# Kernel tuning notes

Hardware: AMD Instinct MI355X
Metric: run time of the kernel (lower is better)

The kernel has to match this reference:

```python
import jax, jax.numpy as jnp
import numpy as np


def setup_inputs() -> dict:
    key = jax.random.key(0)
    k1, k2 = jax.random.split(key)
    n_nodes, n_feat, n_edges = 100000, 64, 1600000
    x = jax.random.normal(k1, (n_nodes, n_feat), dtype=jnp.float32)
    edge_index = jax.random.randint(k2, (2, n_edges), 0, n_nodes, dtype=jnp.int64)
    return {"x": x, "edge_index": edge_index}


def reference(x, edge_index):
    # Faithful JAX version of OneHopGCNNormNodeLabelAggregator.forward:
    #   adj = SparseTensor.from_edge_index(edge_index)  (values = 1)
    #   adj_norm = gcn_norm(adj)  -> add self-loops (diag=1), symmetric D^-1/2 A D^-1/2
    #   x_neighbors = adj_norm.t() @ x
    n = x.shape[0]
    self_loops = jnp.arange(n, dtype=edge_index.dtype)
    row = jnp.concatenate([edge_index[0], self_loops])  # source of adj entry A[row, col]
    col = jnp.concatenate([edge_index[1], self_loops])
    # degree over rows (sparsesum dim=1 after fill_diag)
    deg = jax.ops.segment_sum(jnp.ones(row.shape, x.dtype), row, num_segments=n)
    deg_inv_sqrt = jnp.where(deg > 0, jax.lax.rsqrt(deg), 0.0).astype(x.dtype)
    # symmetric norm weight per edge
    w = deg_inv_sqrt[row] * deg_inv_sqrt[col]  # [E+n]
    # adj_norm.t() @ x : out[col] += w * x[row]
    x_neighbors = jax.ops.segment_sum(w[:, None] * x[row], col, num_segments=n)
    return x_neighbors
```

## Files before the change

kernel.cpp:

```cpp
#include <hip/hip_runtime.h>

#define NFEAT 64
#define BSHIFT 8
#define BCOLS 256
#define NBMAX 512
#define CAP 5120
#define CHUNK 4096
#define PT 512
#define NITP (CHUNK / PT)
#define FT 512
#define UT 512
#define FBIT (CAP / UT)


__device__ __forceinline__ unsigned short f2bf(float f) {
    unsigned int u = __float_as_uint(f);
    return (unsigned short)((u + 0x7FFFu + ((u >> 16) & 1u)) >> 16);
}

__device__ __forceinline__ float bflo(unsigned int u) {
    return __uint_as_float(u << 16);
}
__device__ __forceinline__ float bfhi(unsigned int u) {
    return __uint_as_float(u & 0xFFFF0000u);
}

__device__ __forceinline__ int wave_incl_scan(int v, int lane) {
    #pragma unroll
    for (int off = 1; off < 64; off <<= 1) {
        int u = __shfl_up(v, off);
        if (lane >= off) v += u;
    }
    return v;
}

__global__ void k_init(int* __restrict__ bcur, int* __restrict__ bcurR) {
    int t = threadIdx.x;
    bcur[t]  = t * CAP;
    bcurR[t] = t * CAP;
}

__global__ __launch_bounds__(PT)
void k_partCR(const int* __restrict__ rows, const int* __restrict__ cols,
              int* __restrict__ bcur, int* __restrict__ bcurR,
              int* __restrict__ part, unsigned char* __restrict__ partR, int E) {
    __shared__ int histC[NBMAX];
    __shared__ int histR[NBMAX];
    __shared__ int gbaseC[NBMAX];
    __shared__ int gbaseR[NBMAX];
    __shared__ int wsumC[8];
    __shared__ int wsumR[8];
    __shared__ int stageC[CHUNK];
    __shared__ unsigned char stageR[CHUNK];
    __shared__ unsigned short bidC[CHUNK];
    __shared__ unsigned short bidR[CHUNK];
    int chunk0 = blockIdx.x * CHUNK;
    int cnt = min(CHUNK, E - chunk0);
    int t = threadIdx.x;
    int lane = t & 63, wid = t >> 6;

    histC[t] = 0; histR[t] = 0;
    __syncthreads();

    int pk[NITP];
    unsigned char rpk[NITP];
    unsigned short cb[NITP], rb[NITP];
    #pragma unroll
    for (int k = 0; k < NITP; k++) {
        int i = t + k * PT;
        if (i < cnt) {
            int c = cols[chunk0 + i];
            int r = rows[chunk0 + i];
            int b  = c >> BSHIFT;
            int b2 = r >> BSHIFT;
            pk[k]  = ((c & (BCOLS - 1)) << 17) | r;
            rpk[k] = (unsigned char)(r & (BCOLS - 1));
            cb[k] = (unsigned short)b;
            rb[k] = (unsigned short)b2;
            atomicAdd(&histC[b], 1);
            atomicAdd(&histR[b2], 1);
        }
    }
    __syncthreads();

    int v1 = histC[t];
    int inc1 = wave_incl_scan(v1, lane);
    if (lane == 63) wsumC[wid] = inc1;
    int v2 = histR[t];
    int inc2 = wave_incl_scan(v2, lane);
    if (lane == 63) wsumR[wid] = inc2;
    __syncthreads();
    int addC = 0, addR = 0;
    #pragma unroll
    for (int k = 0; k < 8; k++) {
        if (k < wid) { addC += wsumC[k]; addR += wsumR[k]; }
    }
    int exC = inc1 - v1 + addC;
    int exR = inc2 - v2 + addR;
    gbaseC[t] = (v1 > 0) ? (atomicAdd(&bcur[t], v1) - exC) : 0;
    gbaseR[t] = (v2 > 0) ? (atomicAdd(&bcurR[t], v2) - exR) : 0;
    histC[t] = exC;
    histR[t] = exR;
    __syncthreads();

    #pragma unroll
    for (int k = 0; k < NITP; k++) {
        int i = t + k * PT;
        if (i < cnt) {
            int p = atomicAdd(&histC[cb[k]], 1);
            stageC[p] = pk[k];
            bidC[p] = cb[k];
            int p2 = atomicAdd(&histR[rb[k]], 1);
            stageR[p2] = rpk[k];
            bidR[p2] = rb[k];
        }
    }
    __syncthreads();
    for (int p = t; p < cnt; p += PT) {
        int b = bidC[p];
        int idx = gbaseC[b] + p;
        if (idx < (b + 1) * CAP) part[idx] = stageC[p];
        int b2 = bidR[p];
        int idx2 = gbaseR[b2] + p;
        if (idx2 < (b2 + 1) * CAP) partR[idx2] = stageR[p];
    }
}

__global__ __launch_bounds__(FT)
void k_fillR(const unsigned char* __restrict__ partR, const int* __restrict__ bcurR,
             const float4* __restrict__ x4, float* __restrict__ dinv,
             ushort4* __restrict__ xs4, int n) {
    __shared__ int lcnt[BCOLS];
    __shared__ float ldinv[BCOLS];
    int b = blockIdx.x;
    int s = b * CAP;
    int t = threadIdx.x;

    int cntR = min(bcurR[b] - s, CAP);
    if (t < BCOLS) lcnt[t] = 0;
    __syncthreads();
    for (int i = t; i < cntR; i += FT)
        atomicAdd(&lcnt[partR[s + i]], 1);
    __syncthreads();
    if (t < BCOLS) {
        float d = rsqrtf((float)(lcnt[t] + 1));
        ldinv[t] = d;
        int gr = (b << BSHIFT) + t;
        if (gr < n) dinv[gr] = d;
    }
    __syncthreads();
    size_t base4 = (size_t)(b << BSHIFT) << 4;
    int lim = min(BCOLS, n - (b << BSHIFT)) << 4;
    for (int i = t; i < lim; i += FT) {
        float dd = ldinv[i >> 4];
        float4 vv = x4[base4 + i];
        ushort4 o;
        o.x = f2bf(dd * vv.x); o.y = f2bf(dd * vv.y);
        o.z = f2bf(dd * vv.z); o.w = f2bf(dd * vv.w);
        xs4[base4 + i] = o;
    }
}

__global__ __launch_bounds__(UT)
void k_fuse(const int* __restrict__ part, const int* __restrict__ bcur,
            const unsigned short* __restrict__ xs,
            const float* __restrict__ dinv,
            float4* __restrict__ out4, int n) {
    __shared__ int lcnt[BCOLS];
    __shared__ int lps[BCOLS];
    __shared__ int cur[BCOLS];
    __shared__ int wsum[4];
    __shared__ int stage[CAP];
    int b = blockIdx.x;
    int s = b * CAP;
    int cnt = min(bcur[b] - s, CAP);
    int t = threadIdx.x;
    int lane = t & 63, wid = t >> 6;

    if (t < BCOLS) lcnt[t] = 0;
    __syncthreads();

    int pk[FBIT];
    #pragma unroll
    for (int k = 0; k < FBIT; k++) {
        int i = t + k * UT;
        if (i < cnt) {
            int v2 = part[s + i];
            pk[k] = v2;
            atomicAdd(&lcnt[v2 >> 17], 1);
        }
    }
    __syncthreads();

    int v = 0, inc = 0;
    if (t < BCOLS) {
        v = lcnt[t];
        inc = wave_incl_scan(v, lane);
        if (lane == 63) wsum[wid] = inc;
    }
    __syncthreads();
    if (t < BCOLS) {
        int add = 0;
        if (wid > 0) add += wsum[0];
        if (wid > 1) add += wsum[1];
        if (wid > 2) add += wsum[2];
        int ex = inc - v + add;
        lps[t] = ex;
        cur[t] = ex;
    }
    __syncthreads();

    #pragma unroll
    for (int k = 0; k < FBIT; k++) {
        int i = t + k * UT;
        if (i < cnt) {
            int v2 = pk[k];
            int p = atomicAdd(&cur[v2 >> 17], 1);
            stage[p] = v2 & 0x1FFFF;
        }
    }
    __syncthreads();

    int gg = t >> 3, li = t & 7;
    #pragma unroll
    for (int cc = 0; cc < BCOLS; cc += 64) {
        int c = cc + gg;
        int node = (b << BSHIFT) + c;
        if (node < n) {
            int ss = lps[c];
            int len = lcnt[c];
            float a0 = 0.f, a1 = 0.f, a2 = 0.f, a3 = 0.f;
            float a4 = 0.f, a5 = 0.f, a6 = 0.f, a7 = 0.f;
            int npair = len >> 1;
            uint4 u0, u1;
            if (npair > 0) {
                int r0 = stage[ss], r1 = stage[ss + 1];
                u0 = *((const uint4*)(xs + ((size_t)r0 << 6)) + li);
                u1 = *((const uint4*)(xs + ((size_t)r1 << 6)) + li);
            }
            for (int q = 1; q < npair; q++) {
                int p = ss + q * 2;
                int r0 = stage[p], r1 = stage[p + 1];
                uint4 n0 = *((const uint4*)(xs + ((size_t)r0 << 6)) + li);
                uint4 n1 = *((const uint4*)(xs + ((size_t)r1 << 6)) + li);
                a0 += bflo(u0.x); a1 += bfhi(u0.x);
                a2 += bflo(u0.y); a3 += bfhi(u0.y);
                a4 += bflo(u0.z); a5 += bfhi(u0.z);
                a6 += bflo(u0.w); a7 += bfhi(u0.w);
                a0 += bflo(u1.x); a1 += bfhi(u1.x);
                a2 += bflo(u1.y); a3 += bfhi(u1.y);
                a4 += bflo(u1.z); a5 += bfhi(u1.z);
                a6 += bflo(u1.w); a7 += bfhi(u1.w);
                u0 = n0; u1 = n1;
            }
            if (npair > 0) {
                a0 += bflo(u0.x); a1 += bfhi(u0.x);
                a2 += bflo(u0.y); a3 += bfhi(u0.y);
                a4 += bflo(u0.z); a5 += bfhi(u0.z);
                a6 += bflo(u0.w); a7 += bfhi(u0.w);
                a0 += bflo(u1.x); a1 += bfhi(u1.x);
                a2 += bflo(u1.y); a3 += bfhi(u1.y);
                a4 += bflo(u1.z); a5 += bfhi(u1.z);
                a6 += bflo(u1.w); a7 += bfhi(u1.w);
            }
            if (len & 1) {
                int r = stage[ss + len - 1];
                uint4 u = *((const uint4*)(xs + ((size_t)r << 6)) + li);
                a0 += bflo(u.x); a1 += bfhi(u.x);
                a2 += bflo(u.y); a3 += bfhi(u.y);
                a4 += bflo(u.z); a5 += bfhi(u.z);
                a6 += bflo(u.w); a7 += bfhi(u.w);
            }
            float dc = dinv[node];
            uint4 us = *((const uint4*)(xs + ((size_t)node << 6)) + li);
            float4 r0o, r1o;
            r0o.x = dc * (a0 + bflo(us.x));
            r0o.y = dc * (a1 + bfhi(us.x));
            r0o.z = dc * (a2 + bflo(us.y));
            r0o.w = dc * (a3 + bfhi(us.y));
            r1o.x = dc * (a4 + bflo(us.z));
            r1o.y = dc * (a5 + bfhi(us.z));
            r1o.z = dc * (a6 + bflo(us.w));
            r1o.w = dc * (a7 + bfhi(us.w));
            size_t ob = ((size_t)node << 4) + (li << 1);
            out4[ob] = r0o;
            out4[ob + 1] = r1o;
        }
    }
}

extern "C" void kernel_launch(void* const* d_in, const int* in_sizes, int n_in,
                              void* d_out, int out_size, void* d_ws, size_t ws_size,
                              hipStream_t stream) {
    const float* x    = (const float*)d_in[0];
    const int*   eidx = (const int*)d_in[1];

    const int n = in_sizes[0] / NFEAT;
    const int E = in_sizes[1] / 2;
    const int* rows = eidx;
    const int* cols = eidx + E;
    float* out = (float*)d_out;

    const int nbuck = (n + BCOLS - 1) >> BSHIFT;

    char* w = (char*)d_ws;
    int*   bcur  = (int*)w;     w += NBMAX * 4;
    int*   bcurR = (int*)w;     w += NBMAX * 4;
    float* dinv  = (float*)w;   w += (size_t)n * 4;
    w = (char*)(((uintptr_t)w + 15) & ~(uintptr_t)15);
    unsigned short* xs = (unsigned short*)w;  w += (size_t)n * NFEAT * 2;
    int*   part  = (int*)w;     w += (size_t)nbuck * CAP * 4;
    unsigned char* partR = (unsigned char*)w;

    k_init<<<1, NBMAX, 0, stream>>>(bcur, bcurR);

    int nchunk = (E + CHUNK - 1) / CHUNK;
    k_partCR<<<nchunk, PT, 0, stream>>>(rows, cols, bcur, bcurR, part, partR, E);
    k_fillR<<<nbuck, FT, 0, stream>>>(partR, bcurR, (const float4*)x,
                                      dinv, (ushort4*)xs, n);
    k_fuse<<<nbuck, UT, 0, stream>>>(part, bcur, xs, dinv,
                                     (float4*)out, n);
}
```

Baseline: 140.5 us.

## Replace shared-memory atomics with wave ballot match-based histogram and ranking

Replaces per-element LDS atomicAdd in the partition, degree-count and bucket-sort kernels with a ballot-based key-matching scheme. Each wave computes an equality mask over the bucket bits, keeps per-wave histograms, and places each element by its rank within the mask, so no atomics are needed inside the wave. This targets LDS atomic contention and serialization. In exchange it adds 8-9 ballots per key, larger per-wave shared arrays, and register-held masks.

```diff
diff --git a/kernel.cpp b/kernel.cpp
--- a/kernel.cpp
+++ b/kernel.cpp
@@ -25,6 +25,18 @@
     return __uint_as_float(u & 0xFFFF0000u);
 }
 
+template <int NB>
+__device__ __forceinline__ unsigned long long eqmask(int key,
+                                                     unsigned long long act) {
+    unsigned long long m = act;
+    #pragma unroll
+    for (int b = 0; b < NB; b++) {
+        unsigned long long bb = __ballot((key >> b) & 1);
+        m &= ((key >> b) & 1) ? bb : ~bb;
+    }
+    return m;
+}
+
 __device__ __forceinline__ int wave_incl_scan(int v, int lane) {
     #pragma unroll
     for (int off = 1; off < 64; off <<= 1) {
@@ -44,8 +56,8 @@
 void k_partCR(const int* __restrict__ rows, const int* __restrict__ cols,
               int* __restrict__ bcur, int* __restrict__ bcurR,
               int* __restrict__ part, unsigned char* __restrict__ partR, int E) {
-    __shared__ int histC[NBMAX];
-    __shared__ int histR[NBMAX];
+    __shared__ int cwC[8][NBMAX];
+    __shared__ int cwR[8][NBMAX];
     __shared__ int gbaseC[NBMAX];
     __shared__ int gbaseR[NBMAX];
     __shared__ int wsumC[8];
@@ -58,35 +70,40 @@
     int cnt = min(CHUNK, E - chunk0);
     int t = threadIdx.x;
     int lane = t & 63, wid = t >> 6;
-
-    histC[t] = 0; histR[t] = 0;
-    __syncthreads();
-
-    int pk[NITP];
-    unsigned char rpk[NITP];
-    unsigned short cb[NITP], rb[NITP];
+    unsigned long long lowm = (1ULL << lane) - 1ULL;
+
+    for (int i = t; i < 8 * NBMAX; i += PT) ((int*)cwC)[i] = 0;
+    for (int i = t; i < 8 * NBMAX; i += PT) ((int*)cwR)[i] = 0;
+    __syncthreads();
+
+    int pk[NITP], cb[NITP];
+    unsigned long long mC[NITP], mR[NITP];
     #pragma unroll
     for (int k = 0; k < NITP; k++) {
         int i = t + k * PT;
-        if (i < cnt) {
-            int c = cols[chunk0 + i];
-            int r = rows[chunk0 + i];
-            int b  = c >> BSHIFT;
-            int b2 = r >> BSHIFT;
-            pk[k]  = ((c & (BCOLS - 1)) << 17) | r;
-            rpk[k] = (unsigned char)(r & (BCOLS - 1));
-            cb[k] = (unsigned short)b;
-            rb[k] = (unsigned short)b2;
-            atomicAdd(&histC[b], 1);
-            atomicAdd(&histR[b2], 1);
+        bool valid = i < cnt;
+        int c = 0, r = 0;
+        if (valid) { c = cols[chunk0 + i]; r = rows[chunk0 + i]; }
+        int b  = c >> BSHIFT;
+        int b2 = r >> BSHIFT;
+        pk[k] = ((c & (BCOLS - 1)) << 17) | r;
+        cb[k] = b;
+        unsigned long long act = __ballot(valid);
+        unsigned long long mc = eqmask<9>(b, act);
+        unsigned long long mr = eqmask<9>(b2, act);
+        mC[k] = mc; mR[k] = mr;
+        if (valid) {
+            if (__popcll(mc & lowm) == 0) cwC[wid][b]  += __popcll(mc);
+            if (__popcll(mr & lowm) == 0) cwR[wid][b2] += __popcll(mr);
         }
     }
     __syncthreads();
 
-    int v1 = histC[t];
+    int v1 = 0, v2 = 0;
+    #pragma unroll
+    for (int w = 0; w < 8; w++) { v1 += cwC[w][t]; v2 += cwR[w][t]; }
     int inc1 = wave_incl_scan(v1, lane);
     if (lane == 63) wsumC[wid] = inc1;
-    int v2 = histR[t];
     int inc2 = wave_incl_scan(v2, lane);
     if (lane == 63) wsumR[wid] = inc2;
     __syncthreads();
@@ -99,23 +116,38 @@
     int exR = inc2 - v2 + addR;
     gbaseC[t] = (v1 > 0) ? (atomicAdd(&bcur[t], v1) - exC) : 0;
     gbaseR[t] = (v2 > 0) ? (atomicAdd(&bcurR[t], v2) - exR) : 0;
-    histC[t] = exC;
-    histR[t] = exR;
+    int run = exC;
+    #pragma unroll
+    for (int w = 0; w < 8; w++) { int tmp = cwC[w][t]; cwC[w][t] = run; run += tmp; }
+    run = exR;
+    #pragma unroll
+    for (int w = 0; w < 8; w++) { int tmp = cwR[w][t]; cwR[w][t] = run; run += tmp; }
     __syncthreads();
 
     #pragma unroll
     for (int k = 0; k < NITP; k++) {
         int i = t + k * PT;
-        if (i < cnt) {
-            int p = atomicAdd(&histC[cb[k]], 1);
+        bool valid = i < cnt;
+        unsigned long long mc = mC[k], mr = mR[k];
+        if (valid) {
+            int b = cb[k];
+            int rkC = __popcll(mc & lowm);
+            int curC = cwC[wid][b];
+            int p = curC + rkC;
             stageC[p] = pk[k];
-            bidC[p] = cb[k];
-            int p2 = atomicAdd(&histR[rb[k]], 1);
-            stageR[p2] = rpk[k];
-            bidR[p2] = rb[k];
+            bidC[p] = (unsigned short)b;
+            if (rkC == 0) cwC[wid][b] = curC + __popcll(mc);
+            int b2 = (pk[k] >> 8) & 511;
+            int rkR = __popcll(mr & lowm);
+            int curR = cwR[wid][b2];
+            int p2 = curR + rkR;
+            stageR[p2] = (unsigned char)(pk[k] & 255);
+            bidR[p2] = (unsigned short)b2;
+            if (rkR == 0) cwR[wid][b2] = curR + __popcll(mr);
         }
     }
     __syncthreads();
+
     for (int p = t; p < cnt; p += PT) {
         int b = bidC[p];
         int idx = gbaseC[b] + p;
@@ -130,23 +162,35 @@
 void k_fillR(const unsigned char* __restrict__ partR, const int* __restrict__ bcurR,
              const float4* __restrict__ x4, float* __restrict__ dinv,
              ushort4* __restrict__ xs4, int n) {
-    __shared__ int lcnt[BCOLS];
+    __shared__ int cw[8][BCOLS];
     __shared__ float ldinv[BCOLS];
     int b = blockIdx.x;
     int s = b * CAP;
     int t = threadIdx.x;
+    int lane = t & 63, wid = t >> 6;
+    unsigned long long lowm = (1ULL << lane) - 1ULL;
 
     int cntR = min(bcurR[b] - s, CAP);
-    if (t < BCOLS) lcnt[t] = 0;
-    __syncthreads();
-    for (int i = t; i < cntR; i += FT)
-        atomicAdd(&lcnt[partR[s + i]], 1);
+    for (int i = t; i < 8 * BCOLS; i += FT) ((int*)cw)[i] = 0;
+    __syncthreads();
+    for (int base = 0; base < cntR; base += FT) {
+        int i = base + t;
+        bool valid = i < cntR;
+        int key = 0;
+        if (valid) key = partR[s + i];
+        unsigned long long act = __ballot(valid);
+        unsigned long long m = eqmask<8>(key, act);
+        if (valid && __popcll(m & lowm) == 0) cw[wid][key] += __popcll(m);
+    }
     __syncthreads();
     if (t < BCOLS) {
-        float d = rsqrtf((float)(lcnt[t] + 1));
-        ldinv[t] = d;
+        int d = 0;
+        #pragma unroll
+        for (int w = 0; w < 8; w++) d += cw[w][t];
+        float di = rsqrtf((float)(d + 1));
+        ldinv[t] = di;
         int gr = (b << BSHIFT) + t;
-        if (gr < n) dinv[gr] = d;
+        if (gr < n) dinv[gr] = di;
     }
     __syncthreads();
     size_t base4 = (size_t)(b << BSHIFT) << 4;
@@ -166,9 +210,9 @@
             const unsigned short* __restrict__ xs,
             const float* __restrict__ dinv,
             float4* __restrict__ out4, int n) {
+    __shared__ int cw[8][BCOLS];
     __shared__ int lcnt[BCOLS];
     __shared__ int lps[BCOLS];
-    __shared__ int cur[BCOLS];
     __shared__ int wsum[4];
     __shared__ int stage[CAP];
     int b = blockIdx.x;
@@ -176,25 +220,30 @@
     int cnt = min(bcur[b] - s, CAP);
     int t = threadIdx.x;
     int lane = t & 63, wid = t >> 6;
-
-    if (t < BCOLS) lcnt[t] = 0;
+    unsigned long long lowm = (1ULL << lane) - 1ULL;
+
+    for (int i = t; i < 8 * BCOLS; i += UT) ((int*)cw)[i] = 0;
     __syncthreads();
 
     int pk[FBIT];
     #pragma unroll
     for (int k = 0; k < FBIT; k++) {
         int i = t + k * UT;
-        if (i < cnt) {
-            int v2 = part[s + i];
-            pk[k] = v2;
-            atomicAdd(&lcnt[v2 >> 17], 1);
-        }
+        bool valid = i < cnt;
+        int v2 = 0;
+        if (valid) v2 = part[s + i];
+        pk[k] = v2;
+        int c = v2 >> 17;
+        unsigned long long act = __ballot(valid);
+        unsigned long long m = eqmask<8>(c, act);
+        if (valid && __popcll(m & lowm) == 0) cw[wid][c] += __popcll(m);
     }
     __syncthreads();
 
     int v = 0, inc = 0;
     if (t < BCOLS) {
-        v = lcnt[t];
+        #pragma unroll
+        for (int w = 0; w < 8; w++) v += cw[w][t];
         inc = wave_incl_scan(v, lane);
         if (lane == 63) wsum[wid] = inc;
     }
@@ -206,17 +255,26 @@
         if (wid > 2) add += wsum[2];
         int ex = inc - v + add;
         lps[t] = ex;
-        cur[t] = ex;
+        lcnt[t] = v;
+        int run = ex;
+        #pragma unroll
+        for (int w = 0; w < 8; w++) { int tmp = cw[w][t]; cw[w][t] = run; run += tmp; }
     }
     __syncthreads();
 
     #pragma unroll
     for (int k = 0; k < FBIT; k++) {
         int i = t + k * UT;
-        if (i < cnt) {
-            int v2 = pk[k];
-            int p = atomicAdd(&cur[v2 >> 17], 1);
-            stage[p] = v2 & 0x1FFFF;
+        bool valid = i < cnt;
+        int v2 = pk[k];
+        int c = v2 >> 17;
+        unsigned long long act = __ballot(valid);
+        unsigned long long m = eqmask<8>(c, act);
+        if (valid) {
+            int rk = __popcll(m & lowm);
+            int cur = cw[wid][c];
+            stage[cur + rk] = v2 & 0x1FFFF;
+            if (rk == 0) cw[wid][c] = cur + __popcll(m);
         }
     }
     __syncthreads();
```

After: 166.4 us. 1.18x slower.

## Split fill and fuse blocks into sub-bucket slices for more parallelism

Applied to the files above, without the earlier changes.

Each bucket is now handled by several blocks: k_fillR splits a bucket into two 128-row halves and k_fuse into four 64-column quarters. Each block rescans the whole bucket's partition and keeps only its slice. With only about 391 buckets, the old one-block-per-bucket grid left the GPU underfilled and each block walked four columns sequentially. The cost is redundant reads of the partition data, and a new QCAP clamp on the fuse staging buffer that can silently drop edges if one quarter overflows. The partition chunk size also changes, giving more partition blocks.

```diff
diff --git a/kernel.cpp b/kernel.cpp
--- a/kernel.cpp
+++ b/kernel.cpp
@@ -5,12 +5,13 @@
 #define BCOLS 256
 #define NBMAX 512
 #define CAP 5120
-#define CHUNK 4096
+#define CHUNK 3136
 #define PT 512
-#define NITP (CHUNK / PT)
+#define NITP 7
 #define FT 512
 #define UT 512
 #define FBIT (CAP / UT)
+#define QCAP 1664
 
 
 __device__ __forceinline__ unsigned short f2bf(float f) {
@@ -130,27 +131,33 @@
 void k_fillR(const unsigned char* __restrict__ partR, const int* __restrict__ bcurR,
              const float4* __restrict__ x4, float* __restrict__ dinv,
              ushort4* __restrict__ xs4, int n) {
-    __shared__ int lcnt[BCOLS];
-    __shared__ float ldinv[BCOLS];
-    int b = blockIdx.x;
+    __shared__ int lcnt[128];
+    __shared__ float ldinv[128];
+    int bh = blockIdx.x;
+    int b = bh >> 1, half = bh & 1;
     int s = b * CAP;
     int t = threadIdx.x;
 
     int cntR = min(bcurR[b] - s, CAP);
-    if (t < BCOLS) lcnt[t] = 0;
-    __syncthreads();
-    for (int i = t; i < cntR; i += FT)
-        atomicAdd(&lcnt[partR[s + i]], 1);
-    __syncthreads();
-    if (t < BCOLS) {
+    if (t < 128) lcnt[t] = 0;
+    __syncthreads();
+    for (int i = t; i < cntR; i += FT) {
+        int key = partR[s + i];
+        if ((key >> 7) == half) atomicAdd(&lcnt[key & 127], 1);
+    }
+    __syncthreads();
+    int rows_base = (b << BSHIFT) + (half << 7);
+    if (t < 128) {
         float d = rsqrtf((float)(lcnt[t] + 1));
         ldinv[t] = d;
-        int gr = (b << BSHIFT) + t;
+        int gr = rows_base + t;
         if (gr < n) dinv[gr] = d;
     }
     __syncthreads();
-    size_t base4 = (size_t)(b << BSHIFT) << 4;
-    int lim = min(BCOLS, n - (b << BSHIFT)) << 4;
+    size_t base4 = (size_t)rows_base << 4;
+    int nr = n - rows_base;
+    if (nr <= 0) return;
+    int lim = min(128, nr) << 4;
     for (int i = t; i < lim; i += FT) {
         float dd = ldinv[i >> 4];
         float4 vv = x4[base4 + i];
@@ -166,45 +173,36 @@
             const unsigned short* __restrict__ xs,
             const float* __restrict__ dinv,
             float4* __restrict__ out4, int n) {
-    __shared__ int lcnt[BCOLS];
-    __shared__ int lps[BCOLS];
-    __shared__ int cur[BCOLS];
-    __shared__ int wsum[4];
-    __shared__ int stage[CAP];
-    int b = blockIdx.x;
+    __shared__ int lcnt[64];
+    __shared__ int lps[64];
+    __shared__ int cur[64];
+    __shared__ int stage[QCAP];
+    int qb = blockIdx.x;
+    int b = qb >> 2, q = qb & 3;
     int s = b * CAP;
     int cnt = min(bcur[b] - s, CAP);
     int t = threadIdx.x;
-    int lane = t & 63, wid = t >> 6;
-
-    if (t < BCOLS) lcnt[t] = 0;
+
+    if (t < 64) lcnt[t] = 0;
     __syncthreads();
 
     int pk[FBIT];
     #pragma unroll
     for (int k = 0; k < FBIT; k++) {
         int i = t + k * UT;
-        if (i < cnt) {
-            int v2 = part[s + i];
-            pk[k] = v2;
-            atomicAdd(&lcnt[v2 >> 17], 1);
+        int v2 = (i < cnt) ? part[s + i] : -1;
+        pk[k] = v2;
+        if (v2 >= 0) {
+            int c = v2 >> 17;
+            if ((c >> 6) == q) atomicAdd(&lcnt[c & 63], 1);
         }
     }
     __syncthreads();
 
-    int v = 0, inc = 0;
-    if (t < BCOLS) {
-        v = lcnt[t];
-        inc = wave_incl_scan(v, lane);
-        if (lane == 63) wsum[wid] = inc;
-    }
-    __syncthreads();
-    if (t < BCOLS) {
-        int add = 0;
-        if (wid > 0) add += wsum[0];
-        if (wid > 1) add += wsum[1];
-        if (wid > 2) add += wsum[2];
-        int ex = inc - v + add;
+    if (t < 64) {
+        int v = lcnt[t];
+        int inc = wave_incl_scan(v, t);
+        int ex = inc - v;
         lps[t] = ex;
         cur[t] = ex;
     }
@@ -212,81 +210,79 @@
 
     #pragma unroll
     for (int k = 0; k < FBIT; k++) {
-        int i = t + k * UT;
-        if (i < cnt) {
-            int v2 = pk[k];
-            int p = atomicAdd(&cur[v2 >> 17], 1);
-            stage[p] = v2 & 0x1FFFF;
+        int v2 = pk[k];
+        if (v2 >= 0) {
+            int c = v2 >> 17;
+            if ((c >> 6) == q) {
+                int p = atomicAdd(&cur[c & 63], 1);
+                if (p < QCAP) stage[p] = v2 & 0x1FFFF;
+            }
         }
     }
     __syncthreads();
 
-    int gg = t >> 3, li = t & 7;
-    #pragma unroll
-    for (int cc = 0; cc < BCOLS; cc += 64) {
-        int c = cc + gg;
-        int node = (b << BSHIFT) + c;
-        if (node < n) {
-            int ss = lps[c];
-            int len = lcnt[c];
-            float a0 = 0.f, a1 = 0.f, a2 = 0.f, a3 = 0.f;
-            float a4 = 0.f, a5 = 0.f, a6 = 0.f, a7 = 0.f;
-            int npair = len >> 1;
-            uint4 u0, u1;
-            if (npair > 0) {
-                int r0 = stage[ss], r1 = stage[ss + 1];
-                u0 = *((const uint4*)(xs + ((size_t)r0 << 6)) + li);
-                u1 = *((const uint4*)(xs + ((size_t)r1 << 6)) + li);
-            }
-            for (int q = 1; q < npair; q++) {
-                int p = ss + q * 2;
-                int r0 = stage[p], r1 = stage[p + 1];
-                uint4 n0 = *((const uint4*)(xs + ((size_t)r0 << 6)) + li);
-                uint4 n1 = *((const uint4*)(xs + ((size_t)r1 << 6)) + li);
-                a0 += bflo(u0.x); a1 += bfhi(u0.x);
-                a2 += bflo(u0.y); a3 += bfhi(u0.y);
-                a4 += bflo(u0.z); a5 += bfhi(u0.z);
-                a6 += bflo(u0.w); a7 += bfhi(u0.w);
-                a0 += bflo(u1.x); a1 += bfhi(u1.x);
-                a2 += bflo(u1.y); a3 += bfhi(u1.y);
-                a4 += bflo(u1.z); a5 += bfhi(u1.z);
-                a6 += bflo(u1.w); a7 += bfhi(u1.w);
-                u0 = n0; u1 = n1;
-            }
-            if (npair > 0) {
-                a0 += bflo(u0.x); a1 += bfhi(u0.x);
-                a2 += bflo(u0.y); a3 += bfhi(u0.y);
-                a4 += bflo(u0.z); a5 += bfhi(u0.z);
-                a6 += bflo(u0.w); a7 += bfhi(u0.w);
-                a0 += bflo(u1.x); a1 += bfhi(u1.x);
-                a2 += bflo(u1.y); a3 += bfhi(u1.y);
-                a4 += bflo(u1.z); a5 += bfhi(u1.z);
-                a6 += bflo(u1.w); a7 += bfhi(u1.w);
-            }
-            if (len & 1) {
-                int r = stage[ss + len - 1];
-                uint4 u = *((const uint4*)(xs + ((size_t)r << 6)) + li);
-                a0 += bflo(u.x); a1 += bfhi(u.x);
-                a2 += bflo(u.y); a3 += bfhi(u.y);
-                a4 += bflo(u.z); a5 += bfhi(u.z);
-                a6 += bflo(u.w); a7 += bfhi(u.w);
-            }
-            float dc = dinv[node];
-            uint4 us = *((const uint4*)(xs + ((size_t)node << 6)) + li);
-            float4 r0o, r1o;
-            r0o.x = dc * (a0 + bflo(us.x));
-            r0o.y = dc * (a1 + bfhi(us.x));
-            r0o.z = dc * (a2 + bflo(us.y));
-            r0o.w = dc * (a3 + bfhi(us.y));
-            r1o.x = dc * (a4 + bflo(us.z));
-            r1o.y = dc * (a5 + bfhi(us.z));
-            r1o.z = dc * (a6 + bflo(us.w));
-            r1o.w = dc * (a7 + bfhi(us.w));
-            size_t ob = ((size_t)node << 4) + (li << 1);
-            out4[ob] = r0o;
-            out4[ob + 1] = r1o;
-        }
-    }
+    int g = t >> 3, li = t & 7;
+    int node = (b << BSHIFT) + (q << 6) + g;
+    if (node >= n) return;
+    int ss = lps[g];
+    int len = lcnt[g];
+    if (ss + len > QCAP) len = QCAP > ss ? QCAP - ss : 0;
+    float a0 = 0.f, a1 = 0.f, a2 = 0.f, a3 = 0.f;
+    float a4 = 0.f, a5 = 0.f, a6 = 0.f, a7 = 0.f;
+    int npair = len >> 1;
+    uint4 u0, u1;
+    if (npair > 0) {
+        int r0 = stage[ss], r1 = stage[ss + 1];
+        u0 = *((const uint4*)(xs + ((size_t)r0 << 6)) + li);
+        u1 = *((const uint4*)(xs + ((size_t)r1 << 6)) + li);
+    }
+    for (int qq = 1; qq < npair; qq++) {
+        int p = ss + qq * 2;
+        int r0 = stage[p], r1 = stage[p + 1];
+        uint4 n0 = *((const uint4*)(xs + ((size_t)r0 << 6)) + li);
+        uint4 n1 = *((const uint4*)(xs + ((size_t)r1 << 6)) + li);
+        a0 += bflo(u0.x); a1 += bfhi(u0.x);
+        a2 += bflo(u0.y); a3 += bfhi(u0.y);
+        a4 += bflo(u0.z); a5 += bfhi(u0.z);
+        a6 += bflo(u0.w); a7 += bfhi(u0.w);
+        a0 += bflo(u1.x); a1 += bfhi(u1.x);
+        a2 += bflo(u1.y); a3 += bfhi(u1.y);
+        a4 += bflo(u1.z); a5 += bfhi(u1.z);
+        a6 += bflo(u1.w); a7 += bfhi(u1.w);
+        u0 = n0; u1 = n1;
+    }
+    if (npair > 0) {
+        a0 += bflo(u0.x); a1 += bfhi(u0.x);
+        a2 += bflo(u0.y); a3 += bfhi(u0.y);
+        a4 += bflo(u0.z); a5 += bfhi(u0.z);
+        a6 += bflo(u0.w); a7 += bfhi(u0.w);
+        a0 += bflo(u1.x); a1 += bfhi(u1.x);
+        a2 += bflo(u1.y); a3 += bfhi(u1.y);
+        a4 += bflo(u1.z); a5 += bfhi(u1.z);
+        a6 += bflo(u1.w); a7 += bfhi(u1.w);
+    }
+    if (len & 1) {
+        int r = stage[ss + len - 1];
+        uint4 u = *((const uint4*)(xs + ((size_t)r << 6)) + li);
+        a0 += bflo(u.x); a1 += bfhi(u.x);
+        a2 += bflo(u.y); a3 += bfhi(u.y);
+        a4 += bflo(u.z); a5 += bfhi(u.z);
+        a6 += bflo(u.w); a7 += bfhi(u.w);
+    }
+    float dc = dinv[node];
+    uint4 us = *((const uint4*)(xs + ((size_t)node << 6)) + li);
+    float4 r0o, r1o;
+    r0o.x = dc * (a0 + bflo(us.x));
+    r0o.y = dc * (a1 + bfhi(us.x));
+    r0o.z = dc * (a2 + bflo(us.y));
+    r0o.w = dc * (a3 + bfhi(us.y));
+    r1o.x = dc * (a4 + bflo(us.z));
+    r1o.y = dc * (a5 + bfhi(us.z));
+    r1o.z = dc * (a6 + bflo(us.w));
+    r1o.w = dc * (a7 + bfhi(us.w));
+    size_t ob = ((size_t)node << 4) + (li << 1);
+    out4[ob] = r0o;
+    out4[ob + 1] = r1o;
 }
 
 extern "C" void kernel_launch(void* const* d_in, const int* in_sizes, int n_in,
@@ -316,8 +312,8 @@
 
     int nchunk = (E + CHUNK - 1) / CHUNK;
     k_partCR<<<nchunk, PT, 0, stream>>>(rows, cols, bcur, bcurR, part, partR, E);
-    k_fillR<<<nbuck, FT, 0, stream>>>(partR, bcurR, (const float4*)x,
-                                      dinv, (ushort4*)xs, n);
-    k_fuse<<<nbuck, UT, 0, stream>>>(part, bcur, xs, dinv,
-                                     (float4*)out, n);
-}
+    k_fillR<<<nbuck * 2, FT, 0, stream>>>(partR, bcurR, (const float4*)x,
+                                          dinv, (ushort4*)xs, n);
+    k_fuse<<<nbuck * 4, UT, 0, stream>>>(part, bcur, xs, dinv,
+                                         (float4*)out, n);
+}
```

New measurement: 143.1 us. About the same (+1.9%).
